# Performance work log

Hardware: AMD Instinct MI355X
Metric: run time of the kernel (lower is better)

The kernel has to match this reference:

```python
import jax, jax.numpy as jnp
import numpy as np

B, H, W = 16, 16, 16
DIM = 768
NH = 8
HD = DIM // NH
NEXP = 8
TOPK = 2
DSTATE = 1
DTRANK = 4
KDIR = 4


def setup_inputs() -> dict:
    key = jax.random.key(0)
    ks = jax.random.split(key, 16)
    s = 1.0 / float(np.sqrt(DIM))
    inp = {
        'x': jax.random.normal(ks[0], (B, H, W, DIM)),
        'sa_in_w': jax.random.normal(ks[1], (3 * DIM, DIM)) * s,
        'sa_in_b': jnp.zeros((3 * DIM,)),
        'sa_out_w': jax.random.normal(ks[2], (DIM, DIM)) * s,
        'sa_out_b': jnp.zeros((DIM,)),
        'ca_in_w': jax.random.normal(ks[3], (2 * DIM, DIM)) * s,
        'ca_in_b': jnp.zeros((2 * DIM,)),
        'expert_queries': jax.random.normal(ks[4], (NEXP, DIM)) * s,
        'e_in_w': jax.random.normal(ks[5], (NEXP, 2 * DIM, DIM)) * s,
        'e_in_b': jnp.zeros((NEXP, 2 * DIM)),
        'e_conv_w': jax.random.normal(ks[6], (NEXP, DIM, 1, 3, 3)) / 3.0,
        'e_conv_b': jnp.zeros((NEXP, DIM)),
        'e_xproj_w': jax.random.normal(ks[7], (NEXP, KDIR, DTRANK + 2 * DSTATE, DIM)) * s,
        'e_dtproj_w': jax.random.normal(ks[8], (NEXP, KDIR, DIM, DTRANK)) * 0.1,
        'e_dtproj_b': jax.random.uniform(ks[9], (NEXP, KDIR, DIM), minval=-4.0, maxval=-2.0),
        'e_Alog': jax.random.uniform(ks[10], (NEXP, KDIR, DIM, DSTATE), minval=0.0, maxval=1.0),
        'e_D': jnp.ones((NEXP, KDIR, DIM)),
        'e_ln_scale': jnp.ones((NEXP, DIM)),
        'e_ln_bias': jnp.zeros((NEXP, DIM)),
    }
    return {k: v.astype(jnp.float32) for k, v in inp.items()}


def _selective_scan(xs, Wx, Wdt, bdt, Alog, D):
    # xs: [B, L, d]; Wx: [R+2N, d]; Wdt: [d, R]; Alog: [d, N]; D: [d]
    dbl = jnp.einsum('bld,ed->ble', xs, Wx)
    dt = jax.nn.softplus(jnp.einsum('blr,dr->bld', dbl[..., :DTRANK], Wdt) + bdt)
    Bm = dbl[..., DTRANK:DTRANK + DSTATE]
    Cm = dbl[..., DTRANK + DSTATE:]
    A = -jnp.exp(Alog)  # [d, N]

    def step(h, t):
        dt_t, B_t, C_t, x_t = t  # [b,d],[b,N],[b,N],[b,d]
        h = jnp.exp(dt_t[:, :, None] * A) * h + (dt_t * x_t)[:, :, None] * B_t[:, None, :]
        return h, jnp.einsum('bdn,bn->bd', h, C_t)

    b, L, d = xs.shape
    h0 = jnp.zeros((b, d, DSTATE), xs.dtype)
    tm = lambda a: jnp.moveaxis(a, 1, 0)
    _, ys = jax.lax.scan(step, h0, (tm(dt), tm(Bm), tm(Cm), tm(xs)))
    return jnp.moveaxis(ys, 0, 1) + D * xs


def _expert(in_w, in_b, conv_w, conv_b, xproj_w, dtp_w, dtp_b, Alog, D, ln_s, ln_b, x):
    b = x.shape[0]
    xz = jnp.einsum('bhwc,oc->bhwo', x, in_w) + in_b
    xc, z = jnp.split(xz, 2, axis=-1)
    xn = jax.lax.conv_general_dilated(jnp.transpose(xc, (0, 3, 1, 2)), conv_w,
                                      (1, 1), ((1, 1), (1, 1)), feature_group_count=DIM)
    xc = jax.nn.silu(jnp.transpose(xn + conv_b[None, :, None, None], (0, 2, 3, 1)))
    L = H * W
    xh = xc.reshape(b, L, DIM)                              # row-major 'h'
    xv = jnp.transpose(xc, (0, 2, 1, 3)).reshape(b, L, DIM)  # col-major 'v'
    seqs = jnp.stack([xh, xh[:, ::-1], xv, xv[:, ::-1]])     # [4, b, L, d]
    ys = jax.vmap(_selective_scan)(seqs, xproj_w, dtp_w, dtp_b, Alog, D)
    yv = ys[2] + ys[3][:, ::-1]
    yv = jnp.transpose(yv.reshape(b, W, H, DIM), (0, 2, 1, 3)).reshape(b, L, DIM)
    y = (ys[0] + ys[1][:, ::-1] + yv).reshape(b, H, W, DIM)
    mu = y.mean(-1, keepdims=True)
    var = ((y - mu) ** 2).mean(-1, keepdims=True)
    y = (y - mu) * jax.lax.rsqrt(var + 1e-5) * ln_s + ln_b   # out_norm (LayerNorm)
    y = y * jax.nn.silu(z)
    return y.mean((1, 2))  # AdaptiveAvgPool2d((1,1)) -> [b, DIM]


def _forward(x, sa_in_w, sa_in_b, sa_out_w, sa_out_b, ca_in_w, ca_in_b, expert_queries,
             e_in_w, e_in_b, e_conv_w, e_conv_b, e_xproj_w, e_dtproj_w, e_dtproj_b,
             e_Alog, e_D, e_ln_scale, e_ln_bias):
    b = x.shape[0]
    L = H * W
    scale = 1.0 / float(np.sqrt(HD))
    xs = x.reshape(b, L, DIM)
    # spatial self-attention (eval mode: dropout off)
    qkv = xs @ sa_in_w.T + sa_in_b
    q, k, v = [a.reshape(b, L, NH, HD) for a in jnp.split(qkv, 3, -1)]
    att = jax.nn.softmax(jnp.einsum('bqhd,bkhd->bhqk', q, k) * scale, -1)
    ctx = jnp.einsum('bhqk,bkhd->bqhd', att, v).reshape(b, L, DIM) @ sa_out_w.T + sa_out_b
    # expert cross-attention: only head-averaged attention weights are used
    q2 = (ctx @ ca_in_w[:DIM].T + ca_in_b[:DIM]).reshape(b, L, NH, HD)
    k2 = (expert_queries @ ca_in_w[DIM:].T + ca_in_b[DIM:]).reshape(NEXP, NH, HD)
    aw = jax.nn.softmax(jnp.einsum('blhd,ehd->bhle', q2, k2) * scale, -1).mean(1)  # [b,L,E]
    gate = jax.nn.softmax(aw.mean(1), -1)  # [b, E]
    tk_scores, tk_idx = jax.lax.top_k(gate, TOPK)
    wgt = jax.nn.softmax(tk_scores, -1)
    # dense expert compute (all experts on all samples), then gather top-k
    all_out = jax.vmap(_expert, in_axes=(0,) * 11 + (None,))(
        e_in_w, e_in_b, e_conv_w, e_conv_b, e_xproj_w, e_dtproj_w, e_dtproj_b,
        e_Alog, e_D, e_ln_scale, e_ln_bias, x)  # [E, b, DIM]
    per_b = jnp.transpose(all_out, (1, 0, 2))  # [b, E, DIM]
    sel = jnp.take_along_axis(per_b, tk_idx[:, :, None], axis=1)  # [b, K, DIM]
    return jnp.sum(wgt[:, :, None] * sel, axis=1)  # [b, DIM]


def reference(x, sa_in_w, sa_in_b, sa_out_w, sa_out_b, ca_in_w, ca_in_b, expert_queries,
              e_in_w, e_in_b, e_conv_w, e_conv_b, e_xproj_w, e_dtproj_w, e_dtproj_b,
              e_Alog, e_D, e_ln_scale, e_ln_bias):
    return _forward(x, sa_in_w, sa_in_b, sa_out_w, sa_out_b, ca_in_w, ca_in_b, expert_queries,
                    e_in_w, e_in_b, e_conv_w, e_conv_b, e_xproj_w, e_dtproj_w, e_dtproj_b,
                    e_Alog, e_D, e_ln_scale, e_ln_bias)
```

## Files before the change

kernel.cpp:

```cpp
#include <hip/hip_runtime.h>
#include <hip/hip_bf16.h>


#define LTOK 256
#define DIMC 768

typedef unsigned short ushortt;
typedef __attribute__((ext_vector_type(8))) short bf16x8;
typedef __attribute__((ext_vector_type(4))) float f32x4;

#define LOG2E 1.44269504f
#define LN2   0.69314718f

__device__ __forceinline__ void gld16(const ushortt* gp, ushortt* lp) {
  __builtin_amdgcn_global_load_lds(
      (const __attribute__((address_space(1))) void*)gp,
      (__attribute__((address_space(3))) void*)lp, 16, 0, 0);
}

__device__ __forceinline__ float fexp2(float x) { return __builtin_amdgcn_exp2f(x); }
__device__ __forceinline__ float flog2(float x) { return __builtin_amdgcn_logf(x); }

__device__ __forceinline__ ushortt f2b(float f) {
  union { float f; unsigned u; } c; c.f = f;
  unsigned r = (c.u + 0x7FFFu + ((c.u >> 16) & 1u)) >> 16;
  return (ushortt)r;
}

__global__ __launch_bounds__(256) void mk_mcast4(
    const float* __restrict__ s0, ushortt* __restrict__ d0,
    const float* __restrict__ s1, ushortt* __restrict__ d1,
    const float* __restrict__ s2, ushortt* __restrict__ d2,
    const float* __restrict__ s3, ushortt* __restrict__ d3,
    float* __restrict__ gacc)
{
  if (blockIdx.x == 0 && threadIdx.x < 128) gacc[threadIdx.x] = 0.f;
  long g = (long)blockIdx.x * 256 + threadIdx.x;
  const float* s; ushortt* dst; long o;
  if (g < 786432)       { s = s0; dst = d0; o = g; }
  else if (g < 1228800) { s = s1; dst = d1; o = g - 786432; }
  else if (g < 1376256) { s = s2; dst = d2; o = g - 1228800; }
  else                  { s = s3; dst = d3; o = g - 1376256; }
  o <<= 2;
  float4 v = *(const float4*)(s + o);
  ushort4 w;
  w.x = f2b(v.x); w.y = f2b(v.y); w.z = f2b(v.z); w.w = f2b(v.w);
  *(ushort4*)(dst + o) = w;
}

__global__ __launch_bounds__(256) void mk_cast(const float* __restrict__ in,
                                               ushortt* __restrict__ outp, long n)
{
  long i = ((long)blockIdx.x * 256 + threadIdx.x) * 4;
  if (i + 3 < n) {
    float4 v = *(const float4*)(in + i);
    ushort4 o;
    o.x = f2b(v.x); o.y = f2b(v.y); o.z = f2b(v.z); o.w = f2b(v.w);
    *(ushort4*)(outp + i) = o;
  }
}

__global__ __launch_bounds__(256) void mk_mfma(
    const ushortt* __restrict__ A, const ushortt* __restrict__ B,
    const float* __restrict__ bias, void* __restrict__ C,
    int K, int lda, int ldb, int ldc,
    int zdiv, long sA1, long sA2, long sB1, long sB2, long sC1, long sC2,
    long sBias,
    const int* __restrict__ pairExp, int tilesN,
    int outBf, int splitN, void* __restrict__ C2, int ldc2, int outBf2, int c2vt)
{
  int z = blockIdx.y;
  long aoff, boff, coff, biasoff = 0;
  if (pairExp) {
    int e = pairExp[z];
    aoff = (long)(z >> 1) * sA1; boff = (long)e * sB1;
    coff = (long)z * sC1; biasoff = (long)e * sBias;
  } else {
    int z1 = z / zdiv, z2 = z - z1 * zdiv;
    aoff = (long)z1 * sA1 + (long)z2 * sA2;
    boff = (long)z1 * sB1 + (long)z2 * sB2;
    coff = (long)z1 * sC1 + (long)z2 * sC2;
  }
  int tile = blockIdx.x;
  int tm = tile / tilesN, tn = tile - tm * tilesN;
  long m0 = (long)tm << 7, n0 = (long)tn << 7;

  __shared__ ushortt As[128 * 32];
  __shared__ ushortt Bs[128 * 32];

  int tid = threadIdx.x;
  int lane = tid & 63, wvi = tid >> 6;
  int wr = wvi >> 1, wc = wvi & 1;
  int lm = lane & 15, lg = lane >> 4;

  f32x4 zero4 = {0.f, 0.f, 0.f, 0.f};
  f32x4 acc[4][4];
#pragma unroll
  for (int i = 0; i < 4; i++)
#pragma unroll
    for (int j = 0; j < 4; j++) acc[i][j] = zero4;

  const ushortt* Ab = A + aoff;
  const ushortt* Bb = B + boff;

  int srow = (wvi << 5) + (lane >> 2);
  int sglog = ((lane & 3) ^ ((lane >> 3) & 3)) << 3;
  const ushortt* agp = Ab + (m0 + srow) * lda + sglog;
  const ushortt* bgp = Bb + (n0 + srow) * ldb + sglog;
  ushortt* al0 = &As[(wvi << 5) << 5];
  ushortt* al1 = &As[((wvi << 5) + 16) << 5];
  ushortt* bl0 = &Bs[(wvi << 5) << 5];
  ushortt* bl1 = &Bs[((wvi << 5) + 16) << 5];

  int pswz = (lg ^ ((lm >> 1) & 3)) << 3;
  const ushortt* afp[4];
  const ushortt* bfp[4];
#pragma unroll
  for (int i = 0; i < 4; i++) {
    afp[i] = &As[((wr * 64 + i * 16 + lm) << 5) + pswz];
    bfp[i] = &Bs[((wc * 64 + i * 16 + lm) << 5) + pswz];
  }

  for (int k0 = 0; k0 < K; k0 += 32) {
    gld16(agp, al0);
    gld16(agp + 16 * lda, al1);
    gld16(bgp, bl0);
    gld16(bgp + 16 * ldb, bl1);
    agp += 32; bgp += 32;
    __syncthreads();
    bf16x8 af[4], bfr[4];
#pragma unroll
    for (int i = 0; i < 4; i++) {
      af[i] = *(const bf16x8*)afp[i];
      bfr[i] = *(const bf16x8*)bfp[i];
    }
#pragma unroll
    for (int i = 0; i < 4; i++)
#pragma unroll
      for (int j = 0; j < 4; j++)
        acc[i][j] = __builtin_amdgcn_mfma_f32_16x16x32_bf16(af[i], bfr[j], acc[i][j], 0, 0, 0);
    __syncthreads();
  }

#pragma unroll
  for (int mt = 0; mt < 4; mt++) {
#pragma unroll
    for (int nt = 0; nt < 4; nt++) {
      long grow = m0 + wr * 64 + mt * 16 + lg * 4;
      long gcol = n0 + wc * 64 + nt * 16 + lm;
      float bv = bias ? bias[biasoff + gcol] : 0.f;
      if ((int)gcol < splitN) {
#pragma unroll
        for (int r = 0; r < 4; r++) {
          float v = acc[mt][nt][r] + bv;
          long idx = coff + (grow + r) * ldc + gcol;
          if (outBf) ((ushortt*)C)[idx] = f2b(v);
          else ((float*)C)[idx] = v;
        }
      } else if (c2vt) {
        int cc = (int)gcol - splitN;
        int hh = cc / 96, jj = cc - hh * 96;
#pragma unroll
        for (int r = 0; r < 4; r++) {
          float v = acc[mt][nt][r] + bv;
          long gr = grow + r;
          long b = gr >> 8, t = gr & 255;
          long idx = (((b * 8 + hh) * 128 + jj) << 8) + t;
          ((ushortt*)C2)[idx] = f2b(v);
        }
      } else {
        long col = gcol - splitN;
#pragma unroll
        for (int r = 0; r < 4; r++) {
          float v = acc[mt][nt][r] + bv;
          long idx = coff + (grow + r) * ldc2 + col;
          if (outBf2) ((ushortt*)C2)[idx] = f2b(v);
          else ((float*)C2)[idx] = v;
        }
      }
    }
  }
}

__global__ __launch_bounds__(256) void mk_attv(const float* __restrict__ scores,
                                               const ushortt* __restrict__ vt,
                                               ushortt* __restrict__ ctxa)
{
  __shared__ ushortt Vs[96 * 264];
  __shared__ __attribute__((aligned(16))) ushortt As[128 * 40];
  int z = blockIdx.y, half = blockIdx.x;
  int t = threadIdx.x;
  const float* srow = scores + (long)z * 65536 + (long)half * 128 * 256;
  const ushortt* vb = vt + (long)z * 32768;

  for (int it = 0; it < 12; it++) {
    int cch = it * 256 + t;
    int j = cch >> 5, q = cch & 31;
    *(uint4*)&Vs[j * 264 + q * 8] = *(const uint4*)(vb + j * 256 + q * 8);
  }

  int r = t >> 1, hf = t & 1;
  const float* sp = srow + (long)r * 256 + hf * 128;
  const float sl = 0.10206207261596577f * LOG2E;
  float m = -3.4e38f;
  for (int j = 0; j < 128; j += 4) {
    float4 v = *(const float4*)(sp + j);
    m = fmaxf(m, fmaxf(fmaxf(v.x, v.y), fmaxf(v.z, v.w)));
  }
  m = fmaxf(m, __shfl_xor(m, 1, 64));
  float s = 0.f;
  for (int j = 0; j < 128; j += 4) {
    float4 v = *(const float4*)(sp + j);
    s += fexp2(sl * (v.x - m)) + fexp2(sl * (v.y - m)) +
         fexp2(sl * (v.z - m)) + fexp2(sl * (v.w - m));
  }
  s += __shfl_xor(s, 1, 64);
  float rinv = 1.f / s;

  int lane = t & 63, w = t >> 6;
  int lm = lane & 15, lg = lane >> 4;
  f32x4 zero4 = {0.f, 0.f, 0.f, 0.f};
  f32x4 acc[2][6];
#pragma unroll
  for (int i = 0; i < 2; i++)
#pragma unroll
    for (int j = 0; j < 6; j++) acc[i][j] = zero4;

  const float* stp = srow + (long)(t >> 1) * 256 + (t & 1) * 16;
  ushortt* adst = &As[(t >> 1) * 40 + (t & 1) * 16];

  for (int k0 = 0; k0 < 256; k0 += 32) {
    float4 a0 = *(const float4*)(stp + k0);
    float4 a1 = *(const float4*)(stp + k0 + 4);
    float4 a2 = *(const float4*)(stp + k0 + 8);
    float4 a3 = *(const float4*)(stp + k0 + 12);
    ushortt pk[16];
    pk[0]  = f2b(fexp2(sl * (a0.x - m)) * rinv);
    pk[1]  = f2b(fexp2(sl * (a0.y - m)) * rinv);
    pk[2]  = f2b(fexp2(sl * (a0.z - m)) * rinv);
    pk[3]  = f2b(fexp2(sl * (a0.w - m)) * rinv);
    pk[4]  = f2b(fexp2(sl * (a1.x - m)) * rinv);
    pk[5]  = f2b(fexp2(sl * (a1.y - m)) * rinv);
    pk[6]  = f2b(fexp2(sl * (a1.z - m)) * rinv);
    pk[7]  = f2b(fexp2(sl * (a1.w - m)) * rinv);
    pk[8]  = f2b(fexp2(sl * (a2.x - m)) * rinv);
    pk[9]  = f2b(fexp2(sl * (a2.y - m)) * rinv);
    pk[10] = f2b(fexp2(sl * (a2.z - m)) * rinv);
    pk[11] = f2b(fexp2(sl * (a2.w - m)) * rinv);
    pk[12] = f2b(fexp2(sl * (a3.x - m)) * rinv);
    pk[13] = f2b(fexp2(sl * (a3.y - m)) * rinv);
    pk[14] = f2b(fexp2(sl * (a3.z - m)) * rinv);
    pk[15] = f2b(fexp2(sl * (a3.w - m)) * rinv);
    *(uint4*)adst = *(uint4*)&pk[0];
    *(uint4*)(adst + 8) = *(uint4*)&pk[8];
    __syncthreads();
    bf16x8 af[2], bfr[6];
#pragma unroll
    for (int i = 0; i < 2; i++)
      af[i] = *(const bf16x8*)&As[(w * 32 + i * 16 + lm) * 40 + lg * 8];
#pragma unroll
    for (int j = 0; j < 6; j++)
      bfr[j] = *(const bf16x8*)&Vs[(j * 16 + lm) * 264 + k0 + lg * 8];
#pragma unroll
    for (int i = 0; i < 2; i++)
#pragma unroll
      for (int j = 0; j < 6; j++)
        acc[i][j] = __builtin_amdgcn_mfma_f32_16x16x32_bf16(af[i], bfr[j], acc[i][j], 0, 0, 0);
    __syncthreads();
  }

  int b = z >> 3, h = z & 7;
#pragma unroll
  for (int i = 0; i < 2; i++) {
#pragma unroll
    for (int j = 0; j < 6; j++) {
      int tok = half * 128 + w * 32 + i * 16 + lg * 4;
      int col = j * 16 + lm;
#pragma unroll
      for (int rr2 = 0; rr2 < 4; rr2++) {
        ctxa[((long)(b * 256 + tok + rr2)) * 768 + h * 96 + col] = f2b(acc[i][j][rr2]);
      }
    }
  }
}

__global__ __launch_bounds__(256) void mk_gemm(
    const float* __restrict__ A, const float* __restrict__ B,
    const float* __restrict__ bias, float* __restrict__ C,
    int M, int N, int K, int lda, int ldb, int ldc, int tilesN)
{
  int tile = blockIdx.x;
  int tm = tile / tilesN, tn = tile - tm * tilesN;
  int m0 = tm << 6, n0 = tn << 6;

  __shared__ float As[16][68];
  __shared__ float Bs[16][68];

  int tid = threadIdx.x;
  int tx = tid & 15, ty = tid >> 4;
  int lrow = tid >> 2;
  int lk = (tid & 3) << 2;

  float acc[4][4];
#pragma unroll
  for (int i = 0; i < 4; i++)
#pragma unroll
    for (int j = 0; j < 4; j++) acc[i][j] = 0.f;

  for (int k0 = 0; k0 < K; k0 += 16) {
    {
      int gm = m0 + lrow;
      float4 v = {0.f, 0.f, 0.f, 0.f};
      if (gm < M) v = *(const float4*)(A + (long)gm * lda + (k0 + lk));
      As[lk + 0][lrow] = v.x; As[lk + 1][lrow] = v.y;
      As[lk + 2][lrow] = v.z; As[lk + 3][lrow] = v.w;
    }
    {
      int gn = n0 + lrow;
      float4 v = {0.f, 0.f, 0.f, 0.f};
      if (gn < N) v = *(const float4*)(B + (long)gn * ldb + (k0 + lk));
      Bs[lk + 0][lrow] = v.x; Bs[lk + 1][lrow] = v.y;
      Bs[lk + 2][lrow] = v.z; Bs[lk + 3][lrow] = v.w;
    }
    __syncthreads();
#pragma unroll
    for (int kk = 0; kk < 16; kk++) {
      float4 a = *(const float4*)&As[kk][ty << 2];
      float4 b = *(const float4*)&Bs[kk][tx << 2];
      acc[0][0] += a.x * b.x; acc[0][1] += a.x * b.y; acc[0][2] += a.x * b.z; acc[0][3] += a.x * b.w;
      acc[1][0] += a.y * b.x; acc[1][1] += a.y * b.y; acc[1][2] += a.y * b.z; acc[1][3] += a.y * b.w;
      acc[2][0] += a.z * b.x; acc[2][1] += a.z * b.y; acc[2][2] += a.z * b.z; acc[2][3] += a.z * b.w;
      acc[3][0] += a.w * b.x; acc[3][1] += a.w * b.y; acc[3][2] += a.w * b.z; acc[3][3] += a.w * b.w;
    }
    __syncthreads();
  }

#pragma unroll
  for (int i = 0; i < 4; i++) {
    int gm = m0 + (ty << 2) + i;
    if (gm >= M) continue;
#pragma unroll
    for (int j = 0; j < 4; j++) {
      int gn = n0 + (tx << 2) + j;
      if (gn >= N) continue;
      float v = acc[i][j];
      if (bias) v += bias[gn];
      C[(long)gm * ldc + gn] = v;
    }
  }
}

__global__ __launch_bounds__(256) void mk_gates(const float* __restrict__ q2,
                                                const float* __restrict__ k2,
                                                float* __restrict__ gacc)
{
  __shared__ float k2p[8 * 808];
  int b = blockIdx.x >> 4, q = blockIdx.x & 15;
  for (int i = threadIdx.x; i < 6144; i += 256) {
    int e = i / 768, rem = i - e * 768;
    int h = rem / 96, j = rem - h * 96;
    k2p[e * 808 + h * 100 + j] = k2[i];
  }
  __syncthreads();
  const float scale = 0.10206207261596577f;
  int wid = threadIdx.x >> 6, lane = threadIdx.x & 63;
  int h = lane >> 3, e = lane & 7;
  const float* kp = &k2p[e * 808 + h * 100];
  float accL = 0.f;
#pragma unroll
  for (int ti = 0; ti < 4; ti++) {
    int l = q * 16 + wid * 4 + ti;
    const float* qh = q2 + ((long)b * LTOK + l) * DIMC + h * 96;
    float sum = 0.f;
#pragma unroll
    for (int j = 0; j < 96; j += 4) {
      float4 qv = *(const float4*)(qh + j);
      float4 kv = *(const float4*)(kp + j);
      sum += qv.x * kv.x + qv.y * kv.y + qv.z * kv.z + qv.w * kv.w;
    }
    float s = sum * scale;
    float mx = s;
#pragma unroll
    for (int o = 1; o <= 4; o <<= 1) mx = fmaxf(mx, __shfl_xor(mx, o, 64));
    float ex = fexp2((s - mx) * LOG2E);
    float se = ex;
#pragma unroll
    for (int o = 1; o <= 4; o <<= 1) se += __shfl_xor(se, o, 64);
    accL += ex / se;
  }
#pragma unroll
  for (int o = 8; o <= 32; o <<= 1) accL += __shfl_xor(accL, o, 64);
  __shared__ float red[4][8];
  if (lane < 8) red[wid][lane] = accL;
  __syncthreads();
  if (threadIdx.x < 8) {
    float v = red[0][threadIdx.x] + red[1][threadIdx.x] +
              red[2][threadIdx.x] + red[3][threadIdx.x];
    atomicAdd(&gacc[b * 8 + threadIdx.x], v);
  }
}

__global__ __launch_bounds__(64) void mk_gatetop(const float* __restrict__ gacc,
                                                 int* __restrict__ pe,
                                                 float* __restrict__ pw)
{
  int b = threadIdx.x;
  if (b >= 16) return;
  float g[8];
  for (int e = 0; e < 8; e++) g[e] = gacc[b * 8 + e] * (1.f / (8.f * 256.f));
  float mx = g[0];
  for (int e = 1; e < 8; e++) mx = fmaxf(mx, g[e]);
  float se = 0.f;
  for (int e = 0; e < 8; e++) { g[e] = expf(g[e] - mx); se += g[e]; }
  for (int e = 0; e < 8; e++) g[e] /= se;
  int i0 = 0;
  for (int e = 1; e < 8; e++) if (g[e] > g[i0]) i0 = e;
  int i1 = (i0 == 0) ? 1 : 0;
  for (int e = 0; e < 8; e++) if (e != i0 && g[e] > g[i1]) i1 = e;
  float w0 = 1.f / (1.f + expf(g[i1] - g[i0]));
  pe[2 * b] = i0; pe[2 * b + 1] = i1;
  pw[2 * b] = w0; pw[2 * b + 1] = 1.f - w0;
}

__global__ __launch_bounds__(768) void mk_conv(const float* __restrict__ xzx,
                                               const float* __restrict__ cw,
                                               const float* __restrict__ cb,
                                               const int* __restrict__ pe,
                                               float* __restrict__ xc)
{
  int blk = blockIdx.x;
  int p = blk >> 5, tg = blk & 31;
  int e = pe[p];
  int c = threadIdx.x;
  const float* wp = cw + ((long)e * DIMC + c) * 9;
  float w9[9];
#pragma unroll
  for (int i = 0; i < 9; i++) w9[i] = wp[i];
  float bias = cb[e * DIMC + c];
  const float* xb = xzx + (long)p * LTOK * DIMC + c;
#pragma unroll
  for (int i = 0; i < 8; i++) {
    int t = tg * 8 + i;
    int h = t >> 4, w = t & 15;
    float acc = bias;
#pragma unroll
    for (int dh = 0; dh < 3; dh++) {
      int hh = h + dh - 1;
      if (hh < 0 || hh > 15) continue;
#pragma unroll
      for (int dw = 0; dw < 3; dw++) {
        int ww = w + dw - 1;
        if (ww < 0 || ww > 15) continue;
        acc += xb[(long)(hh * 16 + ww) * DIMC] * w9[dh * 3 + dw];
      }
    }
    xc[((long)p * LTOK + t) * DIMC + c] = acc / (1.f + fexp2(-acc * LOG2E));
  }
}

__device__ __forceinline__ int tmap(int dir, int s) {
  if (dir == 0) return s;
  if (dir == 1) return 255 - s;
  if (dir == 2) return ((s & 15) << 4) | (s >> 4);
  int u = 255 - s;
  return ((u & 15) << 4) | (u >> 4);
}

__global__ __launch_bounds__(256) void mk_dbl(const float* __restrict__ xc,
                                              const float* __restrict__ xproj,
                                              const int* __restrict__ pe,
                                              float* __restrict__ dblm,
                                              float* __restrict__ eo)
{
  if (blockIdx.x < 96) eo[blockIdx.x * 256 + threadIdx.x] = 0.f;
  int p = blockIdx.x >> 6;
  int tq = blockIdx.x & 63;
  int wid = threadIdx.x >> 6, lane = threadIdx.x & 63;
  int m = tq * 4 + wid;
  int e = pe[p];
  const float* xr = xc + ((long)p * LTOK + m) * DIMC;
  const float* wb = xproj + (long)e * 24 * DIMC;
  float4 xv[3];
#pragma unroll
  for (int j = 0; j < 3; j++) xv[j] = *(const float4*)(xr + j * 256 + lane * 4);
  float acc[24];
#pragma unroll
  for (int r = 0; r < 24; r++) {
    const float* wr = wb + r * DIMC;
    float s = 0.f;
#pragma unroll
    for (int j = 0; j < 3; j++) {
      float4 wv = *(const float4*)(wr + j * 256 + lane * 4);
      s += xv[j].x * wv.x + xv[j].y * wv.y + xv[j].z * wv.z + xv[j].w * wv.w;
    }
    acc[r] = s;
  }
#pragma unroll
  for (int r = 0; r < 24; r++)
#pragma unroll
    for (int o = 32; o; o >>= 1) acc[r] += __shfl_xor(acc[r], o, 64);
  if (lane == 0) {
    float* o = dblm + (long)p * 6144;
#pragma unroll
    for (int dd = 0; dd < 4; dd++) {
      int s = tmap(dd, m);
      int ss = ((s & 31) << 3) | (s >> 5);
      float* oa = o + dd * 1024 + ss * 4;
      oa[0] = acc[dd * 6 + 0]; oa[1] = acc[dd * 6 + 1];
      oa[2] = acc[dd * 6 + 2]; oa[3] = acc[dd * 6 + 3];
      float* ob = o + 4096 + dd * 512 + ss * 2;
      ob[0] = acc[dd * 6 + 4]; ob[1] = acc[dd * 6 + 5];
    }
  }
}

__global__ __launch_bounds__(512, 6) void mk_scan(const float* __restrict__ xc,
                                               const float* __restrict__ dblm,
                                               const float* __restrict__ dtw,
                                               const float* __restrict__ dtb,
                                               const float* __restrict__ Alog,
                                               const float* __restrict__ Dp,
                                               const int* __restrict__ pe,
                                               float* __restrict__ yac)
{
  __shared__ __attribute__((aligned(16))) float dtS[4096];
  __shared__ __attribute__((aligned(16))) float bcS[2048];
  __shared__ float yS[256 * 18];
  __shared__ float ahS[32][16][2];
  __shared__ float dsum[16];
  int blk = blockIdx.x;
  int p = blk / 48, cg = blk - p * 48;
  int c0 = cg << 4;
  int e = pe[p];
  int tid = threadIdx.x;
  {
    const float4* src = (const float4*)(dblm + (long)p * 6144);
    float4* dA = (float4*)dtS;
    for (int i = tid; i < 1024; i += 512) dA[i] = src[i];
    if (tid < 512) ((float4*)bcS)[tid] = src[1024 + tid];
  }
  for (int i = tid; i < 256 * 18; i += 512) yS[i] = 0.f;
  if (tid < 16) {
    float s = 0.f;
#pragma unroll
    for (int dd = 0; dd < 4; dd++) s += Dp[(long)(e * 4 + dd) * DIMC + c0 + tid];
    dsum[tid] = s;
  }
  __syncthreads();

  int c = tid & 15;
  int rr = tid >> 4;
  int seg = rr & 7;
  int dir = rr >> 3;
  int d = c0 + c;
  const float* xcp = xc + (long)p * LTOK * DIMC + d;
  long pb = (long)(e * 4 + dir) * DIMC + d;
  float4 wv = *(const float4*)(dtw + pb * 4);
  wv.x *= LOG2E; wv.y *= LOG2E; wv.z *= LOG2E; wv.w *= LOG2E;
  float bdt = dtb[pb] * LOG2E;
  float Ad = -fexp2(Alog[pb] * LOG2E);
  int t0 = seg << 5;
  const float* dtP = &dtS[(dir << 10) + (seg << 2)];
  const float* bcP = &bcS[(dir << 9) + (seg << 1)];

  float h = 0.f, ap = 1.f;
#pragma unroll 1
  for (int tb = 0; tb < 32; tb += 4) {
#pragma unroll
    for (int u = 0; u < 4; u++) {
      int i = tb + u;
      float4 dv = *(const float4*)(dtP + i * 32);
      float2 bc = *(const float2*)(bcP + i * 16);
      int mm = tmap(dir, t0 + i);
      float xv = xcp[(long)mm * DIMC];
      float xl = wv.x * dv.x + wv.y * dv.y + wv.z * dv.z + wv.w * dv.w + bdt;
      float te = fexp2(xl);
      float g = flog2(1.f + te);
      g = (xl > 86.f) ? xl : g;
      float de = fexp2(g * Ad);
      h = de * h + (g * LN2 * bc.x) * xv;
      ap *= de;
    }
    __builtin_amdgcn_sched_barrier(0);
  }
  ahS[rr][c][0] = ap;
  ahS[rr][c][1] = h;
  __syncthreads();

  float hh = 0.f;
  {
    int base = dir << 3;
    float av[8], hv[8];
#pragma unroll
    for (int j = 0; j < 8; j++) {
      av[j] = ahS[base + j][c][0];
      hv[j] = ahS[base + j][c][1];
    }
#pragma unroll
    for (int j = 0; j < 7; j++)
      if (j < seg) hh = av[j] * hh + hv[j];
  }

#pragma unroll 1
  for (int tb = 0; tb < 32; tb += 4) {
#pragma unroll
    for (int u = 0; u < 4; u++) {
      int i = tb + u;
      float4 dv = *(const float4*)(dtP + i * 32);
      float2 bc = *(const float2*)(bcP + i * 16);
      int mm = tmap(dir, t0 + i);
      float xv = xcp[(long)mm * DIMC];
      float xl = wv.x * dv.x + wv.y * dv.y + wv.z * dv.z + wv.w * dv.w + bdt;
      float te = fexp2(xl);
      float g = flog2(1.f + te);
      g = (xl > 86.f) ? xl : g;
      float de = fexp2(g * Ad);
      hh = de * hh + (g * LN2 * bc.x) * xv;
      atomicAdd(&yS[mm * 18 + c + (((mm >> 5) & 1) << 1)], hh * bc.y);
    }
    __builtin_amdgcn_sched_barrier(0);
  }
  __syncthreads();

  const float* xcb = xc + (long)p * LTOK * DIMC + c0;
  float* yp = yac + (long)p * LTOK * DIMC + c0;
  for (int i = tid; i < 4096; i += 512) {
    int t = i >> 4, cz = i & 15;
    yp[(long)t * DIMC + cz] = yS[t * 18 + cz + (((t >> 5) & 1) << 1)] +
        xcb[(long)t * DIMC + cz] * dsum[cz];
  }
}

__global__ __launch_bounds__(256) void mk_lnfin(const float* __restrict__ yac,
                                                const float* __restrict__ xzz,
                                                const float* __restrict__ lns,
                                                const float* __restrict__ lnb,
                                                const int* __restrict__ pe,
                                                float* __restrict__ eo)
{
  int blk = blockIdx.x;
  int p = blk >> 4, ts = blk & 15;
  int e = pe[p];
  int tid = threadIdx.x;
  int wid = tid >> 6, lane = tid & 63;
  float ls[12], lb[12], acc[12];
#pragma unroll
  for (int i = 0; i < 12; i++) {
    int d = i * 64 + lane;
    ls[i] = lns[e * DIMC + d];
    lb[i] = lnb[e * DIMC + d];
    acc[i] = 0.f;
  }
#pragma unroll
  for (int tt = 0; tt < 4; tt++) {
    int t = ts * 16 + wid * 4 + tt;
    const float* yr = yac + ((long)p * LTOK + t) * DIMC;
    const float* zr = xzz + ((long)p * LTOK + t) * DIMC;
    float v[12];
    float s = 0.f;
#pragma unroll
    for (int i = 0; i < 12; i++) { v[i] = yr[i * 64 + lane]; s += v[i]; }
#pragma unroll
    for (int o = 32; o; o >>= 1) s += __shfl_xor(s, o, 64);
    float mu = s * (1.f / 768.f);
    float sq = 0.f;
#pragma unroll
    for (int i = 0; i < 12; i++) { float dlt = v[i] - mu; sq += dlt * dlt; }
#pragma unroll
    for (int o = 32; o; o >>= 1) sq += __shfl_xor(sq, o, 64);
    float rs = rsqrtf(sq * (1.f / 768.f) + 1e-5f);
#pragma unroll
    for (int i = 0; i < 12; i++) {
      float y = (v[i] - mu) * rs * ls[i] + lb[i];
      float z = zr[i * 64 + lane];
      y *= z / (1.f + fexp2(-z * LOG2E));
      acc[i] += y;
    }
  }
  __shared__ float sacc[768];
  for (int j = tid; j < 768; j += 256) sacc[j] = 0.f;
  __syncthreads();
#pragma unroll
  for (int i = 0; i < 12; i++) atomicAdd(&sacc[i * 64 + lane], acc[i]);
  __syncthreads();
  for (int j = tid; j < 768; j += 256) atomicAdd(&eo[(long)p * DIMC + j], sacc[j]);
}

__global__ __launch_bounds__(768) void mk_out(const float* __restrict__ eo,
                                              const float* __restrict__ pw,
                                              float* __restrict__ out)
{
  int b = blockIdx.x, d = threadIdx.x;
  float v = pw[2 * b] * eo[(long)(2 * b) * DIMC + d] +
            pw[2 * b + 1] * eo[(long)(2 * b + 1) * DIMC + d];
  out[b * DIMC + d] = v * (1.f / 256.f);
}

extern "C" void kernel_launch(void* const* d_in, const int* in_sizes, int n_in,
                              void* d_out, int out_size, void* d_ws, size_t ws_size,
                              hipStream_t stream)
{
  const float* x        = (const float*)d_in[0];
  const float* sa_in_w  = (const float*)d_in[1];
  const float* sa_in_b  = (const float*)d_in[2];
  const float* sa_out_w = (const float*)d_in[3];
  const float* sa_out_b = (const float*)d_in[4];
  const float* ca_in_w  = (const float*)d_in[5];
  const float* ca_in_b  = (const float*)d_in[6];
  const float* eq       = (const float*)d_in[7];
  const float* e_in_w   = (const float*)d_in[8];
  const float* e_in_b   = (const float*)d_in[9];
  const float* e_conv_w = (const float*)d_in[10];
  const float* e_conv_b = (const float*)d_in[11];
  const float* e_xproj  = (const float*)d_in[12];
  const float* e_dtw    = (const float*)d_in[13];
  const float* e_dtb    = (const float*)d_in[14];
  const float* e_Alog   = (const float*)d_in[15];
  const float* e_D      = (const float*)d_in[16];
  const float* e_lns    = (const float*)d_in[17];
  const float* e_lnb    = (const float*)d_in[18];
  float* out = (float*)d_out;

  float* ws = (float*)d_ws;
  ushortt* qk_b   = (ushortt*)(ws + 0);
  float*   scores = ws + 6291456;
  ushortt* ctxa_b = (ushortt*)(ws + 14680064);
  ushortt* vt_b   = (ushortt*)(ws + 18874368);
  ushortt* xb     = (ushortt*)(ws + 20971520);
  ushortt* wqkv_b = (ushortt*)(ws + 22544384);
  ushortt* saow_b = (ushortt*)(ws + 23429120);
  ushortt* caw_b  = (ushortt*)(ws + 23724032);
  ushortt* ctx_b  = (ushortt*)(ws + 0);
  float*   q2     = ws + 1572864;
  float*   k2     = ws + 25165824;
  int*     pe     = (int*)(ws + 25171968);
  float*   pw     = ws + 25172000;
  float*   eo     = ws + 25172032;
  float*   gacc   = ws + 25393216;
  float*   xz_x   = ws + 0;
  float*   xz_z   = ws + 6291456;
  ushortt* ew_b   = (ushortt*)(ws + 12582912);
  float*   xc     = ws + 12582912;
  float*   yac    = ws + 18874368;
  float*   dblm   = ws + 0;

  mk_mcast4<<<5952, 256, 0, stream>>>(x, xb, sa_in_w, wqkv_b, sa_out_w, saow_b,
                                      ca_in_w, caw_b, gacc);
  mk_mfma<<<dim3(576, 1), 256, 0, stream>>>(xb, wqkv_b, sa_in_b, qk_b,
      768, 768, 768, 1536, 1, 0, 0, 0, 0, 0, 0, 0, nullptr, 18,
      1, 1536, vt_b, 0, 1, 1);
  mk_mfma<<<dim3(4, 128), 256, 0, stream>>>(qk_b, qk_b + 768, nullptr, scores,
      96, 1536, 1536, 256, 8, 393216, 96, 393216, 96, 524288, 65536, 0, nullptr, 2,
      0, 1 << 30, nullptr, 0, 0, 0);
  mk_attv<<<dim3(2, 128), 256, 0, stream>>>(scores, vt_b, ctxa_b);
  mk_mfma<<<dim3(192, 1), 256, 0, stream>>>(ctxa_b, saow_b, sa_out_b, ctx_b,
      768, 768, 768, 768, 1, 0, 0, 0, 0, 0, 0, 0, nullptr, 6,
      1, 1 << 30, nullptr, 0, 0, 0);
  mk_cast<<<9216, 256, 0, stream>>>(e_in_w, ew_b, 9437184);
  mk_mfma<<<dim3(192, 1), 256, 0, stream>>>(ctx_b, caw_b, ca_in_b, q2,
      768, 768, 768, 768, 1, 0, 0, 0, 0, 0, 0, 0, nullptr, 6,
      0, 1 << 30, nullptr, 0, 0, 0);
  mk_gemm<<<dim3(12, 1), 256, 0, stream>>>(eq, ca_in_w + 589824, ca_in_b + 768, k2,
      8, 768, 768, 768, 768, 768, 12);
  mk_gates<<<256, 256, 0, stream>>>(q2, k2, gacc);
  mk_gatetop<<<1, 64, 0, stream>>>(gacc, pe, pw);
  mk_mfma<<<dim3(24, 32), 256, 0, stream>>>(xb, ew_b, e_in_b, xz_x,
      768, 768, 768, 768, 1, 196608, 0, 1179648, 0, 196608, 0, 1536, pe, 12,
      0, 768, xz_z, 768, 0, 0);
  mk_conv<<<1024, 768, 0, stream>>>(xz_x, e_conv_w, e_conv_b, pe, xc);
  mk_dbl<<<2048, 256, 0, stream>>>(xc, e_xproj, pe, dblm, eo);
  mk_scan<<<1536, 512, 0, stream>>>(xc, dblm, e_dtw, e_dtb, e_Alog, e_D, pe, yac);
  mk_lnfin<<<512, 256, 0, stream>>>(yac, xz_z, e_lns, e_lnb, pe, eo);
  mk_out<<<16, 768, 0, stream>>>(eo, pw, out);

  (void)in_sizes; (void)n_in; (void)out_size; (void)ws_size;
}
```

Before: 580.1 us.

## Fuse expert-key GEMM, gate scoring and top-k into one kernel; fold output into lnfin

The small k2 GEMM, the gate softmax-mean kernel and the top-k kernel are replaced by a single 16-block kernel per batch that computes the expert keys in shared memory, scores all 256 tokens, and selects the top-2 experts directly, removing atomics and two launches. The final weighted combine is moved into mk_lnfin using a last-block-done counter, removing the mk_out launch. The trade-off is that the gate work now runs on only 16 blocks, and each block recomputes the full k2 projection redundantly, which may cost more time than the launches it saves.

```diff
diff --git a/kernel.cpp b/kernel.cpp
--- a/kernel.cpp
+++ b/kernel.cpp
@@ -31,10 +31,8 @@
     const float* __restrict__ s0, ushortt* __restrict__ d0,
     const float* __restrict__ s1, ushortt* __restrict__ d1,
     const float* __restrict__ s2, ushortt* __restrict__ d2,
-    const float* __restrict__ s3, ushortt* __restrict__ d3,
-    float* __restrict__ gacc)
-{
-  if (blockIdx.x == 0 && threadIdx.x < 128) gacc[threadIdx.x] = 0.f;
+    const float* __restrict__ s3, ushortt* __restrict__ d3)
+{
   long g = (long)blockIdx.x * 256 + threadIdx.x;
   const float* s; ushortt* dst; long o;
   if (g < 786432)       { s = s0; dst = d0; o = g; }
@@ -284,142 +282,101 @@
   }
 }
 
-__global__ __launch_bounds__(256) void mk_gemm(
-    const float* __restrict__ A, const float* __restrict__ B,
-    const float* __restrict__ bias, float* __restrict__ C,
-    int M, int N, int K, int lda, int ldb, int ldc, int tilesN)
-{
-  int tile = blockIdx.x;
-  int tm = tile / tilesN, tn = tile - tm * tilesN;
-  int m0 = tm << 6, n0 = tn << 6;
-
-  __shared__ float As[16][68];
-  __shared__ float Bs[16][68];
-
+__global__ __launch_bounds__(256) void mk_gates16(
+    const float* __restrict__ q2,
+    const float* __restrict__ eq,
+    const float* __restrict__ caw2,
+    const float* __restrict__ cab2,
+    int* __restrict__ pe, float* __restrict__ pw)
+{
+  __shared__ float eqS[8 * 768];
+  __shared__ float k2p[8 * 808];
+  __shared__ float red2[4][8];
+  int b = blockIdx.x;
   int tid = threadIdx.x;
-  int tx = tid & 15, ty = tid >> 4;
-  int lrow = tid >> 2;
-  int lk = (tid & 3) << 2;
-
-  float acc[4][4];
-#pragma unroll
-  for (int i = 0; i < 4; i++)
-#pragma unroll
-    for (int j = 0; j < 4; j++) acc[i][j] = 0.f;
-
-  for (int k0 = 0; k0 < K; k0 += 16) {
-    {
-      int gm = m0 + lrow;
-      float4 v = {0.f, 0.f, 0.f, 0.f};
-      if (gm < M) v = *(const float4*)(A + (long)gm * lda + (k0 + lk));
-      As[lk + 0][lrow] = v.x; As[lk + 1][lrow] = v.y;
-      As[lk + 2][lrow] = v.z; As[lk + 3][lrow] = v.w;
-    }
-    {
-      int gn = n0 + lrow;
-      float4 v = {0.f, 0.f, 0.f, 0.f};
-      if (gn < N) v = *(const float4*)(B + (long)gn * ldb + (k0 + lk));
-      Bs[lk + 0][lrow] = v.x; Bs[lk + 1][lrow] = v.y;
-      Bs[lk + 2][lrow] = v.z; Bs[lk + 3][lrow] = v.w;
-    }
-    __syncthreads();
-#pragma unroll
-    for (int kk = 0; kk < 16; kk++) {
-      float4 a = *(const float4*)&As[kk][ty << 2];
-      float4 b = *(const float4*)&Bs[kk][tx << 2];
-      acc[0][0] += a.x * b.x; acc[0][1] += a.x * b.y; acc[0][2] += a.x * b.z; acc[0][3] += a.x * b.w;
-      acc[1][0] += a.y * b.x; acc[1][1] += a.y * b.y; acc[1][2] += a.y * b.z; acc[1][3] += a.y * b.w;
-      acc[2][0] += a.z * b.x; acc[2][1] += a.z * b.y; acc[2][2] += a.z * b.z; acc[2][3] += a.z * b.w;
-      acc[3][0] += a.w * b.x; acc[3][1] += a.w * b.y; acc[3][2] += a.w * b.z; acc[3][3] += a.w * b.w;
-    }
-    __syncthreads();
-  }
-
-#pragma unroll
-  for (int i = 0; i < 4; i++) {
-    int gm = m0 + (ty << 2) + i;
-    if (gm >= M) continue;
-#pragma unroll
-    for (int j = 0; j < 4; j++) {
-      int gn = n0 + (tx << 2) + j;
-      if (gn >= N) continue;
-      float v = acc[i][j];
-      if (bias) v += bias[gn];
-      C[(long)gm * ldc + gn] = v;
-    }
-  }
-}
-
-__global__ __launch_bounds__(256) void mk_gates(const float* __restrict__ q2,
-                                                const float* __restrict__ k2,
-                                                float* __restrict__ gacc)
-{
-  __shared__ float k2p[8 * 808];
-  int b = blockIdx.x >> 4, q = blockIdx.x & 15;
-  for (int i = threadIdx.x; i < 6144; i += 256) {
-    int e = i / 768, rem = i - e * 768;
-    int h = rem / 96, j = rem - h * 96;
-    k2p[e * 808 + h * 100 + j] = k2[i];
-  }
-  __syncthreads();
+  for (int i = tid; i < 1536; i += 256)
+    ((float4*)eqS)[i] = ((const float4*)eq)[i];
+  __syncthreads();
+#pragma unroll 1
+  for (int nc = 0; nc < 3; nc++) {
+    int n = nc * 256 + tid;
+    const float* wrow = caw2 + (long)n * 768;
+    float cb = cab2[n];
+    float acc[8];
+#pragma unroll
+    for (int e = 0; e < 8; e++) acc[e] = cb;
+#pragma unroll 1
+    for (int k = 0; k < 768; k += 4) {
+      float4 wv = *(const float4*)(wrow + k);
+#pragma unroll
+      for (int e = 0; e < 8; e++) {
+        float4 ev = *(const float4*)&eqS[e * 768 + k];
+        acc[e] += ev.x * wv.x + ev.y * wv.y + ev.z * wv.z + ev.w * wv.w;
+      }
+    }
+    int h = n / 96, j = n - h * 96;
+#pragma unroll
+    for (int e = 0; e < 8; e++) k2p[e * 808 + h * 100 + j] = acc[e];
+  }
+  __syncthreads();
+
   const float scale = 0.10206207261596577f;
-  int wid = threadIdx.x >> 6, lane = threadIdx.x & 63;
-  int h = lane >> 3, e = lane & 7;
-  const float* kp = &k2p[e * 808 + h * 100];
-  float accL = 0.f;
-#pragma unroll
-  for (int ti = 0; ti < 4; ti++) {
-    int l = q * 16 + wid * 4 + ti;
-    const float* qh = q2 + ((long)b * LTOK + l) * DIMC + h * 96;
-    float sum = 0.f;
-#pragma unroll
+  const float* qrow = q2 + ((long)b * LTOK + tid) * DIMC;
+  float acc8[8];
+#pragma unroll
+  for (int e = 0; e < 8; e++) acc8[e] = 0.f;
+#pragma unroll 1
+  for (int h = 0; h < 8; h++) {
+    float s8[8];
+#pragma unroll
+    for (int e = 0; e < 8; e++) s8[e] = 0.f;
+    const float* qh = qrow + h * 96;
+#pragma unroll 1
     for (int j = 0; j < 96; j += 4) {
       float4 qv = *(const float4*)(qh + j);
-      float4 kv = *(const float4*)(kp + j);
-      sum += qv.x * kv.x + qv.y * kv.y + qv.z * kv.z + qv.w * kv.w;
-    }
-    float s = sum * scale;
-    float mx = s;
-#pragma unroll
-    for (int o = 1; o <= 4; o <<= 1) mx = fmaxf(mx, __shfl_xor(mx, o, 64));
-    float ex = fexp2((s - mx) * LOG2E);
-    float se = ex;
-#pragma unroll
-    for (int o = 1; o <= 4; o <<= 1) se += __shfl_xor(se, o, 64);
-    accL += ex / se;
-  }
-#pragma unroll
-  for (int o = 8; o <= 32; o <<= 1) accL += __shfl_xor(accL, o, 64);
-  __shared__ float red[4][8];
-  if (lane < 8) red[wid][lane] = accL;
-  __syncthreads();
-  if (threadIdx.x < 8) {
-    float v = red[0][threadIdx.x] + red[1][threadIdx.x] +
-              red[2][threadIdx.x] + red[3][threadIdx.x];
-    atomicAdd(&gacc[b * 8 + threadIdx.x], v);
-  }
-}
-
-__global__ __launch_bounds__(64) void mk_gatetop(const float* __restrict__ gacc,
-                                                 int* __restrict__ pe,
-                                                 float* __restrict__ pw)
-{
-  int b = threadIdx.x;
-  if (b >= 16) return;
-  float g[8];
-  for (int e = 0; e < 8; e++) g[e] = gacc[b * 8 + e] * (1.f / (8.f * 256.f));
-  float mx = g[0];
-  for (int e = 1; e < 8; e++) mx = fmaxf(mx, g[e]);
-  float se = 0.f;
-  for (int e = 0; e < 8; e++) { g[e] = expf(g[e] - mx); se += g[e]; }
-  for (int e = 0; e < 8; e++) g[e] /= se;
-  int i0 = 0;
-  for (int e = 1; e < 8; e++) if (g[e] > g[i0]) i0 = e;
-  int i1 = (i0 == 0) ? 1 : 0;
-  for (int e = 0; e < 8; e++) if (e != i0 && g[e] > g[i1]) i1 = e;
-  float w0 = 1.f / (1.f + expf(g[i1] - g[i0]));
-  pe[2 * b] = i0; pe[2 * b + 1] = i1;
-  pw[2 * b] = w0; pw[2 * b + 1] = 1.f - w0;
+#pragma unroll
+      for (int e = 0; e < 8; e++) {
+        float4 kv = *(const float4*)&k2p[e * 808 + h * 100 + j];
+        s8[e] += qv.x * kv.x + qv.y * kv.y + qv.z * kv.z + qv.w * kv.w;
+      }
+    }
+    float mx = s8[0] * scale;
+#pragma unroll
+    for (int e = 1; e < 8; e++) mx = fmaxf(mx, s8[e] * scale);
+    float se = 0.f, ex8[8];
+#pragma unroll
+    for (int e = 0; e < 8; e++) { ex8[e] = fexp2((s8[e] * scale - mx) * LOG2E); se += ex8[e]; }
+    float rr = 1.f / se;
+#pragma unroll
+    for (int e = 0; e < 8; e++) acc8[e] += ex8[e] * rr;
+  }
+#pragma unroll
+  for (int e = 0; e < 8; e++)
+#pragma unroll
+    for (int o = 32; o; o >>= 1) acc8[e] += __shfl_xor(acc8[e], o, 64);
+  int wid = tid >> 6, lane = tid & 63;
+  if (lane == 0) {
+#pragma unroll
+    for (int e = 0; e < 8; e++) red2[wid][e] = acc8[e];
+  }
+  __syncthreads();
+  if (tid == 0) {
+    float g[8];
+    for (int e = 0; e < 8; e++)
+      g[e] = (red2[0][e] + red2[1][e] + red2[2][e] + red2[3][e]) * (1.f / (8.f * 256.f));
+    float mx = g[0];
+    for (int e = 1; e < 8; e++) mx = fmaxf(mx, g[e]);
+    float se = 0.f;
+    for (int e = 0; e < 8; e++) { g[e] = expf(g[e] - mx); se += g[e]; }
+    for (int e = 0; e < 8; e++) g[e] /= se;
+    int i0 = 0;
+    for (int e = 1; e < 8; e++) if (g[e] > g[i0]) i0 = e;
+    int i1 = (i0 == 0) ? 1 : 0;
+    for (int e = 0; e < 8; e++) if (e != i0 && g[e] > g[i1]) i1 = e;
+    float w0 = 1.f / (1.f + expf(g[i1] - g[i0]));
+    pe[2 * b] = i0; pe[2 * b + 1] = i1;
+    pw[2 * b] = w0; pw[2 * b + 1] = 1.f - w0;
+  }
 }
 
 __global__ __launch_bounds__(768) void mk_conv(const float* __restrict__ xzx,
@@ -470,9 +427,11 @@
                                               const float* __restrict__ xproj,
                                               const int* __restrict__ pe,
                                               float* __restrict__ dblm,
-                                              float* __restrict__ eo)
+                                              float* __restrict__ eo,
+                                              int* __restrict__ cnt)
 {
   if (blockIdx.x < 96) eo[blockIdx.x * 256 + threadIdx.x] = 0.f;
+  if (blockIdx.x == 96 && threadIdx.x == 0) *cnt = 0;
   int p = blockIdx.x >> 6;
   int tq = blockIdx.x & 63;
   int wid = threadIdx.x >> 6, lane = threadIdx.x & 63;
@@ -636,7 +595,10 @@
                                                 const float* __restrict__ lns,
                                                 const float* __restrict__ lnb,
                                                 const int* __restrict__ pe,
-                                                float* __restrict__ eo)
+                                                float* __restrict__ eo,
+                                                const float* __restrict__ pw,
+                                                float* __restrict__ out,
+                                                int* __restrict__ cnt)
 {
   int blk = blockIdx.x;
   int p = blk >> 4, ts = blk & 15;
@@ -684,16 +646,20 @@
   for (int i = 0; i < 12; i++) atomicAdd(&sacc[i * 64 + lane], acc[i]);
   __syncthreads();
   for (int j = tid; j < 768; j += 256) atomicAdd(&eo[(long)p * DIMC + j], sacc[j]);
-}
-
-__global__ __launch_bounds__(768) void mk_out(const float* __restrict__ eo,
-                                              const float* __restrict__ pw,
-                                              float* __restrict__ out)
-{
-  int b = blockIdx.x, d = threadIdx.x;
-  float v = pw[2 * b] * eo[(long)(2 * b) * DIMC + d] +
-            pw[2 * b + 1] * eo[(long)(2 * b + 1) * DIMC + d];
-  out[b * DIMC + d] = v * (1.f / 256.f);
+
+  __threadfence();
+  __syncthreads();
+  __shared__ int isLast;
+  if (tid == 0) isLast = (atomicAdd(cnt, 1) == 511) ? 1 : 0;
+  __syncthreads();
+  if (isLast) {
+    for (int i = tid; i < 12288; i += 256) {
+      int b2 = i / 768, d = i - b2 * 768;
+      float v0 = atomicAdd(&eo[(long)(2 * b2) * DIMC + d], 0.f);
+      float v1 = atomicAdd(&eo[(long)(2 * b2 + 1) * DIMC + d], 0.f);
+      out[i] = (pw[2 * b2] * v0 + pw[2 * b2 + 1] * v1) * (1.f / 256.f);
+    }
+  }
 }
 
 extern "C" void kernel_launch(void* const* d_in, const int* in_sizes, int n_in,
@@ -732,11 +698,10 @@
   ushortt* caw_b  = (ushortt*)(ws + 23724032);
   ushortt* ctx_b  = (ushortt*)(ws + 0);
   float*   q2     = ws + 1572864;
-  float*   k2     = ws + 25165824;
   int*     pe     = (int*)(ws + 25171968);
   float*   pw     = ws + 25172000;
   float*   eo     = ws + 25172032;
-  float*   gacc   = ws + 25393216;
+  int*     cnt    = (int*)(ws + 25196608);
   float*   xz_x   = ws + 0;
   float*   xz_z   = ws + 6291456;
   ushortt* ew_b   = (ushortt*)(ws + 12582912);
@@ -745,7 +710,7 @@
   float*   dblm   = ws + 0;
 
   mk_mcast4<<<5952, 256, 0, stream>>>(x, xb, sa_in_w, wqkv_b, sa_out_w, saow_b,
-                                      ca_in_w, caw_b, gacc);
+                                      ca_in_w, caw_b);
   mk_mfma<<<dim3(576, 1), 256, 0, stream>>>(xb, wqkv_b, sa_in_b, qk_b,
       768, 768, 768, 1536, 1, 0, 0, 0, 0, 0, 0, 0, nullptr, 18,
       1, 1536, vt_b, 0, 1, 1);
@@ -760,18 +725,15 @@
   mk_mfma<<<dim3(192, 1), 256, 0, stream>>>(ctx_b, caw_b, ca_in_b, q2,
       768, 768, 768, 768, 1, 0, 0, 0, 0, 0, 0, 0, nullptr, 6,
       0, 1 << 30, nullptr, 0, 0, 0);
-  mk_gemm<<<dim3(12, 1), 256, 0, stream>>>(eq, ca_in_w + 589824, ca_in_b + 768, k2,
-      8, 768, 768, 768, 768, 768, 12);
-  mk_gates<<<256, 256, 0, stream>>>(q2, k2, gacc);
-  mk_gatetop<<<1, 64, 0, stream>>>(gacc, pe, pw);
+  mk_gates16<<<16, 256, 0, stream>>>(q2, eq, ca_in_w + 589824, ca_in_b + 768,
+                                     pe, pw);
   mk_mfma<<<dim3(24, 32), 256, 0, stream>>>(xb, ew_b, e_in_b, xz_x,
       768, 768, 768, 768, 1, 196608, 0, 1179648, 0, 196608, 0, 1536, pe, 12,
       0, 768, xz_z, 768, 0, 0);
   mk_conv<<<1024, 768, 0, stream>>>(xz_x, e_conv_w, e_conv_b, pe, xc);
-  mk_dbl<<<2048, 256, 0, stream>>>(xc, e_xproj, pe, dblm, eo);
+  mk_dbl<<<2048, 256, 0, stream>>>(xc, e_xproj, pe, dblm, eo, cnt);
   mk_scan<<<1536, 512, 0, stream>>>(xc, dblm, e_dtw, e_dtb, e_Alog, e_D, pe, yac);
-  mk_lnfin<<<512, 256, 0, stream>>>(yac, xz_z, e_lns, e_lnb, pe, eo);
-  mk_out<<<16, 768, 0, stream>>>(eo, pw, out);
+  mk_lnfin<<<512, 256, 0, stream>>>(yac, xz_z, e_lns, e_lnb, pe, eo, pw, out, cnt);
 
   (void)in_sizes; (void)n_in; (void)out_size; (void)ws_size;
 }
```

Measured after the change: 732.8 us. 1.26x slower.
